# Kernel tuning notes

Hardware: AMD Instinct MI355X
Metric: run time of the kernel (lower is better)

The kernel has to match this reference:

```python
import jax, jax.numpy as jnp
import numpy as np

DIMVEC = 196
POS_LABEL = 98
NBLABELS = 10
M = 128
UNIHIGH = 0.012
BATCH = 8192


def setup_inputs() -> dict:
    key = jax.random.key(0)
    ks = jax.random.split(key, 6)
    # input features: one 2-vector per site, normalized to unit norm (cos/sin style)
    x = jax.random.uniform(ks[0], (BATCH, DIMVEC, 2), dtype=jnp.float32)
    x = x / jnp.linalg.norm(x, axis=-1, keepdims=True)
    # MPS tensors, uniform(0, unihigh) as in the original construct_tensornetwork
    w0 = jax.random.uniform(ks[1], (2, M), dtype=jnp.float32) * UNIHIGH
    w_left = jax.random.uniform(ks[2], (POS_LABEL - 1, 2, M, M), dtype=jnp.float32) * UNIHIGH
    w_label = jax.random.uniform(ks[3], (2, M, M, NBLABELS), dtype=jnp.float32) * UNIHIGH
    w_right = jax.random.uniform(ks[4], (DIMVEC - 2 - POS_LABEL, 2, M, M), dtype=jnp.float32) * UNIHIGH
    w_end = jax.random.uniform(ks[5], (2, M), dtype=jnp.float32) * UNIHIGH
    return {"x": x, "w0": w0, "w_left": w_left, "w_label": w_label,
            "w_right": w_right, "w_end": w_end}


def reference(x, w0, w_left, w_label, w_right, w_end):
    b, d, _ = x.shape
    m = w0.shape[1]

    # left boundary: contract physical leg of site 0 -> [B, m]
    left = x[:, 0, :] @ w0

    # sweep sites 1 .. pos_label-1: left'[b,n] = sum_{p,mm} x[b,p] left[b,mm] W[p,mm,n]
    def lstep(carry, inp):
        W, xi = inp                       # W: [2,m,m], xi: [B,2]
        o = (xi[:, :, None] * carry[:, None, :]).reshape(b, 2 * m)  # [B, 2m]
        return o @ W.reshape(2 * m, m), None                        # GEMM B x 2m x m

    left, _ = jax.lax.scan(lstep, left,
                           (w_left, jnp.swapaxes(x[:, 1:POS_LABEL], 0, 1)))

    # right boundary: contract physical leg of last site -> [B, m]
    right = x[:, -1, :] @ w_end

    # sweep sites dimvec-2 .. pos_label+1 (reverse):
    # right'[b,mm] = sum_{p,n} x[b,p] right[b,n] W[p,mm,n]
    def rstep(carry, inp):
        W, xi = inp
        o = (xi[:, :, None] * carry[:, None, :]).reshape(b, 2 * m)  # [B, 2m]
        Wt = jnp.swapaxes(W, 1, 2).reshape(2 * m, m)                # [p,n,mm] -> [2m, m]
        return o @ Wt, None

    right, _ = jax.lax.scan(rstep, right,
                            (w_right, jnp.swapaxes(x[:, POS_LABEL + 1:d - 1], 0, 1)),
                            reverse=True)

    # label site: contract left bond first (small intermediate [B,2,m,L])
    xl = x[:, POS_LABEL, :]                                   # [B, 2]
    z = jnp.einsum('bm,pmnl->bpnl', left, w_label)             # [B,2,m,L]
    leftL = jnp.einsum('bpnl,bp->bnl', z, xl)                  # [B,m,L]

    # close the chain with the right environment -> [B, nblabels]
    return jnp.einsum('bnl,bn->bl', leftL, right)
```

## Files before the change

kernel.cpp:

```cpp
#include <hip/hip_runtime.h>

#define BATCH 8192
#define MDIM 128
#define NL 10
#define LSTEPS 97
#define RSTEPS 96
#define NSTEPS 193
#define DIM 196
#define POSL 98

typedef _Float16 half8 __attribute__((ext_vector_type(8)));
typedef float float16v __attribute__((ext_vector_type(16)));

#define BARRIER_LGKM() asm volatile("s_waitcnt lgkmcnt(0)\ns_barrier" ::: "memory")

#define MFMA16 __builtin_amdgcn_mfma_f32_32x32x16_f16

__global__ __launch_bounds__(256) void transpose_x(const float* __restrict__ x,
                                                   float2* __restrict__ xT) {
    __shared__ float tx[64][65];
    __shared__ float ty[64][65];
    int p0 = blockIdx.x * 32;
    int b0 = blockIdx.y * 64;
    int tid = threadIdx.x;

    int r = tid >> 2, q = tid & 3;
    const float* src = x + ((size_t)(b0 + r) * DIM + p0 + q * 8) * 2;
#pragma unroll
    for (int j = 0; j < 8; ++j) {
        int pp = q * 8 + j;
        if (p0 + pp < DIM) {
            float2 v = *(const float2*)(src + j * 2);
            tx[r][pp] = v.x;
            ty[r][pp] = v.y;
        }
    }
    __syncthreads();

    int pr = tid >> 3, cb = (tid & 7) * 8;
    if (p0 + pr < DIM) {
        float2* dst = xT + (size_t)(p0 + pr) * BATCH + b0 + cb;
#pragma unroll
        for (int j = 0; j < 8; ++j) {
            float2 v;
            v.x = tx[cb + j][pr];
            v.y = ty[cb + j][pr];
            dst[j] = v;
        }
    }
}

__global__ __launch_bounds__(256) void pack_w(const float* __restrict__ w_left,
                                              const float* __restrict__ w_right,
                                              _Float16* __restrict__ pw) {
    int g = blockIdx.x >> 2;
    int nt = blockIdx.x & 3;
    int tid = threadIdx.x;
    int l = tid & 63;
    int kq = tid >> 6;
    int hi = l >> 5;
    int n = nt * 32 + (l & 31);
#pragma unroll
    for (int p = 0; p < 4; ++p) {
        int kt = p * 4 + kq;
        int k0 = kt * 16 + hi * 8;
        half8 hv;
        if (g < LSTEPS) {
            const float* base = w_left + (size_t)g * 2 * MDIM * MDIM;
#pragma unroll
            for (int j = 0; j < 8; ++j)
                hv[j] = (_Float16)base[(size_t)(k0 + j) * MDIM + n];
        } else {
            int t = g - LSTEPS;
            int s = k0 >> 7;
            int a0 = k0 & 127;
            const float* row = w_right + (size_t)(RSTEPS - 1 - t) * 2 * MDIM * MDIM
                             + (size_t)s * MDIM * MDIM + (size_t)n * MDIM + a0;
#pragma unroll
            for (int j = 0; j < 8; ++j) hv[j] = (_Float16)row[j];
        }
        *(half8*)(pw + (size_t)(g * 64 + nt * 16 + kt) * 512 + l * 8) = hv;
    }
}

__global__ __launch_bounds__(256) void pack_label(const float* __restrict__ w_label,
                                                  _Float16* __restrict__ gp) {
    int ct = blockIdx.x;
    int tid = threadIdx.x;
    int l = tid & 63;
    int kq = tid >> 6;
    int hi = l >> 5;
    int outcol = ct * 32 + (l & 31);
    int n = outcol & 127;
    int lab = outcol >> 7;
#pragma unroll
    for (int p2 = 0; p2 < 4; ++p2) {
        int kt = p2 * 4 + kq;
        int k0 = kt * 16 + hi * 8;
        int p = k0 >> 7;
        int m0 = k0 & 127;
        half8 hv;
#pragma unroll
        for (int j = 0; j < 8; ++j)
            hv[j] = (_Float16)w_label[(((size_t)p * MDIM + m0 + j) * MDIM + n) * NL + lab];
        *(half8*)(gp + (size_t)(ct * 16 + kt) * 512 + l * 8) = hv;
    }
}


#define LD16(dst, p, ofs) \
    asm volatile("global_load_dwordx4 %0, %1, off offset:" ofs : "=v"(dst) : "v"(p))

#define ISSUE_A(DST, PN) do {                                  \
    const char* _p0 = (PN);                                    \
    LD16(DST[0],  _p0, "0");                                   \
    LD16(DST[1],  _p0, "1024");                                \
    LD16(DST[2],  _p0, "2048");                                \
    LD16(DST[3],  _p0, "3072");                                \
    const char* _p1 = _p0 + 4096;                              \
    LD16(DST[4],  _p1, "0");                                   \
    LD16(DST[5],  _p1, "1024");                                \
    LD16(DST[6],  _p1, "2048");                                \
    LD16(DST[7],  _p1, "3072");                                \
    const char* _p2 = _p0 + 8192;                              \
    LD16(DST[8],  _p2, "0");                                   \
    LD16(DST[9],  _p2, "1024");                                \
    LD16(DST[10], _p2, "2048");                                \
    LD16(DST[11], _p2, "3072");                                \
    const char* _p3 = _p0 + 12288;                             \
    LD16(DST[12], _p3, "0");                                   \
    LD16(DST[13], _p3, "1024");                                \
    LD16(DST[14], _p3, "2048");                                \
    LD16(DST[15], _p3, "3072");                                \
} while (0)

#define WAIT_A16() do {                                        \
    asm volatile("s_waitcnt vmcnt(16)" ::: "memory");          \
    __builtin_amdgcn_sched_barrier(0);                         \
} while (0)

#define WAIT_A0() do {                                         \
    asm volatile("s_waitcnt vmcnt(0)" ::: "memory");           \
    __builtin_amdgcn_sched_barrier(0);                         \
} while (0)

#define CHAIN_MFMA_BLOCK(AF, SRC)                                            \
    half8 bf[8];                                                             \
    _Pragma("unroll")                                                        \
    for (int q = 0; q < 8; ++q) {                                            \
        int nb = q * 2 + hi;                                                 \
        int phys = nb ^ (bl & 15);                                           \
        bf[q] = *(const half8*)&cbuf[SRC][row * 128 + phys * 8];             \
    }                                                                        \
    float16v a0 = {}, a1 = {};                                               \
    _Pragma("unroll")                                                        \
    for (int kt = 0; kt < 8; ++kt) {                                         \
        a0 = MFMA16(AF[kt], bf[kt], a0, 0, 0, 0);                            \
        a1 = MFMA16(AF[kt + 8], bf[kt], a1, 0, 0, 0);                        \
    }

#define EPI_RG(DST, XC)                                                      \
    _Pragma("unroll")                                                        \
    for (int rq = 0; rq < 4; ++rq) {                                         \
        int nb = nt * 4 + rq;                                                \
        int phys = nb ^ (bl & 15);                                           \
        union { _Float16 h[4]; uint2 u; } t;                                 \
        _Pragma("unroll")                                                    \
        for (int r = 0; r < 4; ++r)                                          \
            t.h[r] = (_Float16)((XC).x * a0[rq * 4 + r]                      \
                              + (XC).y * a1[rq * 4 + r]);                    \
        *(uint2*)&cbuf[DST][row * 128 + phys * 8 + hi * 4] = t.u;            \
    }

#define FINAL_STORE(XC)                                                      \
    _Pragma("unroll")                                                        \
    for (int r = 0; r < 16; ++r) {                                           \
        int n = nt * 32 + (r & 3) + 8 * (r >> 2) + 4 * hi;                   \
        outT[(size_t)n * BATCH + bbase + row] = (XC).x * a0[r] + (XC).y * a1[r]; \
    }

__global__ __launch_bounds__(512, 2) void chain_mfma(
        const float2* __restrict__ xT, const float* __restrict__ w0,
        const float* __restrict__ w_end, const _Float16* __restrict__ pw,
        float* __restrict__ leftT, float* __restrict__ rightT) {
    __shared__ _Float16 cbuf[2][64 * 128];
    __shared__ float2 xbuf[98][64];

    int bid = blockIdx.x;
    bool is_left = bid < 128;
    int bbase = (is_left ? bid : bid - 128) * 64;
    int tid = threadIdx.x;
    int l = tid & 63;
    int w = tid >> 6;
    int nt = w & 3;
    int rg = w >> 2;
    int bl = l & 31;
    int hi = l >> 5;
    int row = rg * 32 + bl;

    int nsteps = is_left ? LSTEPS : RSTEPS;
    int gbase = is_left ? 0 : LSTEPS;
    int pbase = is_left ? 0 : 98;
    float* outT = is_left ? leftT : rightT;

    for (int i = tid; i < 98 * 64; i += 512) {
        int pos = i >> 6, b = i & 63;
        xbuf[pos][b] = xT[(size_t)(pbase + pos) * BATCH + bbase + b];
    }
    __syncthreads();

    {
        const float* wst = is_left ? w0 : w_end;
        int b = tid >> 3;
        float2 xv0 = xbuf[is_left ? 0 : 97][b];
#pragma unroll
        for (int h = 0; h < 2; ++h) {
            int nb = (tid & 7) * 2 + h;
            half8 hv;
#pragma unroll
            for (int j = 0; j < 8; ++j) {
                int n = nb * 8 + j;
                hv[j] = (_Float16)(xv0.x * wst[n] + xv0.y * wst[MDIM + n]);
            }
            int phys = nb ^ (b & 15);
            *(half8*)&cbuf[0][b * 128 + phys * 8] = hv;
        }
    }

    const char* pwb = (const char*)pw + (size_t)(gbase * 64 + nt * 16) * 1024
                    + (size_t)l * 16;

    __syncthreads();

    half8 A0[16], A1[16];
    ISSUE_A(A0, pwb);

    int npairs = nsteps >> 1;
    bool oddtail = nsteps & 1;
    int last = nsteps - 1;

#pragma unroll 1
    for (int sp = 0; sp < npairs; ++sp) {
        int s0 = 2 * sp;
        {
            ISSUE_A(A1, pwb + (size_t)(s0 + 1) * 65536);
            WAIT_A16();
            int xi = is_left ? (1 + s0) : (96 - s0);
            float2 xc = xbuf[xi][row];
            CHAIN_MFMA_BLOCK(A0, 0)
            EPI_RG(1, xc)
            BARRIER_LGKM();
        }
        {
            int s1 = s0 + 1;
            int pf = (s0 + 2 <= last) ? (s0 + 2) : last;
            ISSUE_A(A0, pwb + (size_t)pf * 65536);
            WAIT_A16();
            int xi = is_left ? (1 + s1) : (96 - s1);
            float2 xc = xbuf[xi][row];
            CHAIN_MFMA_BLOCK(A1, 1)
            if (s1 == last) {
                FINAL_STORE(xc)
            } else {
                EPI_RG(0, xc)
                BARRIER_LGKM();
            }
        }
    }

    if (oddtail) {
        WAIT_A0();
        float2 xc = xbuf[1 + last][row];
        CHAIN_MFMA_BLOCK(A0, 0)
        FINAL_STORE(xc)
    }
}

__global__ __launch_bounds__(256, 2) void label_mfma(
        const float2* __restrict__ xT, const _Float16* __restrict__ gp,
        const float* __restrict__ leftT, const float* __restrict__ rightT,
        float* __restrict__ out) {
    __shared__ _Float16 R[32 * 256];
    __shared__ float pl[4][32][5];
    __shared__ float xl_s[32][2];

    int bx = blockIdx.x;
    int bbase = blockIdx.y * 32;
    int tid = threadIdx.x;
    int l = tid & 63, nt = tid >> 6, bl = l & 31, hi = l >> 5;

    if (tid < 32) {
        const float2 v = xT[(size_t)POSL * BATCH + bbase + tid];
        xl_s[tid][0] = v.x; xl_s[tid][1] = v.y;
    }
    __syncthreads();

#pragma unroll
    for (int q = 0; q < 4; ++q) {
        int id = tid + q * 256;
        int m = id >> 3;
        int b4 = (id & 7) * 4;
        float4 v = *(const float4*)&leftT[(size_t)m * BATCH + bbase + b4];
        float vv[4] = {v.x, v.y, v.z, v.w};
#pragma unroll
        for (int bi = 0; bi < 4; ++bi) {
            int b = b4 + bi;
            int kb0 = m >> 3;
            int ph0 = (kb0 & 16) | ((kb0 ^ b) & 15);
            R[b * 256 + ph0 * 8 + (m & 7)] = (_Float16)(xl_s[b][0] * vv[bi]);
            int kb1 = kb0 + 16;
            int ph1 = (kb1 & 16) | ((kb1 ^ b) & 15);
            R[b * 256 + ph1 * 8 + (m & 7)] = (_Float16)(xl_s[b][1] * vv[bi]);
        }
    }

    float rv[16];
#pragma unroll
    for (int r = 0; r < 16; ++r) {
        int n = nt * 32 + (r & 3) + 8 * (r >> 2) + 4 * hi;
        rv[r] = rightT[(size_t)n * BATCH + bbase + bl];
    }
    __syncthreads();

    half8 rf[16];
#pragma unroll
    for (int kt = 0; kt < 16; ++kt) {
        int kb = kt * 2 + hi;
        int ph = (kb & 16) | ((kb ^ bl) & 15);
        rf[kt] = *(const half8*)&R[bl * 256 + ph * 8];
    }

    int l0 = bx * 5;
    float outv[5];
#pragma unroll
    for (int li = 0; li < 5; ++li) {
        int ct = (l0 + li) * 4 + nt;
        float16v acc = {};
#pragma unroll
        for (int kt = 0; kt < 16; ++kt) {
            half8 a = *(const half8*)(gp + (size_t)(ct * 16 + kt) * 512 + l * 8);
            acc = __builtin_amdgcn_mfma_f32_32x32x16_f16(a, rf[kt], acc, 0, 0, 0);
        }
        float p = 0.f;
#pragma unroll
        for (int r = 0; r < 16; ++r) p += acc[r] * rv[r];
        p += __shfl_xor(p, 32, 64);
        outv[li] = p;
    }
    if (hi == 0) {
#pragma unroll
        for (int li = 0; li < 5; ++li) pl[nt][bl][li] = outv[li];
    }
    __syncthreads();
    if (tid < 160) {
        int b = tid / 5, li = tid % 5;
        out[(size_t)(bbase + b) * NL + l0 + li] =
            pl[0][b][li] + pl[1][b][li] + pl[2][b][li] + pl[3][b][li];
    }
}

extern "C" void kernel_launch(void* const* d_in, const int* in_sizes, int n_in,
                              void* d_out, int out_size, void* d_ws, size_t ws_size,
                              hipStream_t stream) {
    const float* x       = (const float*)d_in[0];
    const float* w0      = (const float*)d_in[1];
    const float* w_left  = (const float*)d_in[2];
    const float* w_label = (const float*)d_in[3];
    const float* w_right = (const float*)d_in[4];
    const float* w_end   = (const float*)d_in[5];

    _Float16* pw = (_Float16*)d_ws;
    _Float16* gp = pw + (size_t)NSTEPS * 64 * 512;
    float* leftT  = (float*)(gp + (size_t)40 * 16 * 512);
    float* rightT = leftT + (size_t)MDIM * BATCH;
    float2* xT    = (float2*)(rightT + (size_t)MDIM * BATCH);

    transpose_x<<<dim3((DIM + 31) / 32, BATCH / 64), 256, 0, stream>>>(x, xT);
    pack_w<<<dim3(NSTEPS * 4), 256, 0, stream>>>(w_left, w_right, pw);
    pack_label<<<dim3(40), 256, 0, stream>>>(w_label, gp);
    chain_mfma<<<dim3(256), 512, 0, stream>>>(xT, w0, w_end, pw, leftT, rightT);
    label_mfma<<<dim3(2, BATCH / 32), 256, 0, stream>>>(xT, gp, leftT, rightT,
                                                        (float*)d_out);
}
```

Before: 253.9 us.

## Stream chain weights into LDS with global_load_lds double-buffered halves

Chain weight fragments no longer go straight into registers, where each wave loaded its own 16 fragments and the two row-group waves fetched the same data. The block now DMAs each step's weight tile into a double-buffered LDS area with global_load_lds, split into two K-halves, and waves read their fragments from LDS. This halves global weight traffic per block and cuts register pressure. The cost is extra barriers per step, extra LDS reads, and a much larger LDS footprint, which may limit residency to one block per CU.

```diff
diff --git a/kernel.cpp b/kernel.cpp
--- a/kernel.cpp
+++ b/kernel.cpp
@@ -13,8 +13,15 @@
 typedef float float16v __attribute__((ext_vector_type(16)));
 
 #define BARRIER_LGKM() asm volatile("s_waitcnt lgkmcnt(0)\ns_barrier" ::: "memory")
+#define BARRIER_PLAIN() asm volatile("s_barrier" ::: "memory")
+#define WAIT_VM4() asm volatile("s_waitcnt vmcnt(4)" ::: "memory")
 
 #define MFMA16 __builtin_amdgcn_mfma_f32_32x32x16_f16
+
+#define GLL16(G, L)                                                          \
+    __builtin_amdgcn_global_load_lds(                                        \
+        (const __attribute__((address_space(1))) unsigned int*)(G),          \
+        (__attribute__((address_space(3))) unsigned int*)(L), 16, 0, 0)
 
 __global__ __launch_bounds__(256) void transpose_x(const float* __restrict__ x,
                                                    float2* __restrict__ xT) {
@@ -108,56 +115,30 @@
 }
 
 
-#define LD16(dst, p, ofs) \
-    asm volatile("global_load_dwordx4 %0, %1, off offset:" ofs : "=v"(dst) : "v"(p))
-
-#define ISSUE_A(DST, PN) do {                                  \
-    const char* _p0 = (PN);                                    \
-    LD16(DST[0],  _p0, "0");                                   \
-    LD16(DST[1],  _p0, "1024");                                \
-    LD16(DST[2],  _p0, "2048");                                \
-    LD16(DST[3],  _p0, "3072");                                \
-    const char* _p1 = _p0 + 4096;                              \
-    LD16(DST[4],  _p1, "0");                                   \
-    LD16(DST[5],  _p1, "1024");                                \
-    LD16(DST[6],  _p1, "2048");                                \
-    LD16(DST[7],  _p1, "3072");                                \
-    const char* _p2 = _p0 + 8192;                              \
-    LD16(DST[8],  _p2, "0");                                   \
-    LD16(DST[9],  _p2, "1024");                                \
-    LD16(DST[10], _p2, "2048");                                \
-    LD16(DST[11], _p2, "3072");                                \
-    const char* _p3 = _p0 + 12288;                             \
-    LD16(DST[12], _p3, "0");                                   \
-    LD16(DST[13], _p3, "1024");                                \
-    LD16(DST[14], _p3, "2048");                                \
-    LD16(DST[15], _p3, "3072");                                \
+#define ISSUE_HALF(SRC_STEP, P, DST) do {                                    \
+    const char* _g = dmasrc + (size_t)(SRC_STEP) * 65536 + (P) * 8192;       \
+    GLL16(_g,        (DST));                                                 \
+    GLL16(_g + 1024, (DST) + 512);                                           \
+    GLL16(_g + 2048, (DST) + 1024);                                          \
+    GLL16(_g + 3072, (DST) + 1536);                                          \
 } while (0)
 
-#define WAIT_A16() do {                                        \
-    asm volatile("s_waitcnt vmcnt(16)" ::: "memory");          \
-    __builtin_amdgcn_sched_barrier(0);                         \
-} while (0)
-
-#define WAIT_A0() do {                                         \
-    asm volatile("s_waitcnt vmcnt(0)" ::: "memory");           \
-    __builtin_amdgcn_sched_barrier(0);                         \
-} while (0)
-
-#define CHAIN_MFMA_BLOCK(AF, SRC)                                            \
-    half8 bf[8];                                                             \
+#define READ_BF(SRC)                                                         \
     _Pragma("unroll")                                                        \
     for (int q = 0; q < 8; ++q) {                                            \
         int nb = q * 2 + hi;                                                 \
         int phys = nb ^ (bl & 15);                                           \
         bf[q] = *(const half8*)&cbuf[SRC][row * 128 + phys * 8];             \
-    }                                                                        \
-    float16v a0 = {}, a1 = {};                                               \
-    _Pragma("unroll")                                                        \
-    for (int kt = 0; kt < 8; ++kt) {                                         \
-        a0 = MFMA16(AF[kt], bf[kt], a0, 0, 0, 0);                            \
-        a1 = MFMA16(AF[kt + 8], bf[kt], a1, 0, 0, 0);                        \
-    }
+    }
+
+#define READ_AF(P)                                                           \
+    _Pragma("unroll")                                                        \
+    for (int f = 0; f < 8; ++f)                                              \
+        af[f] = *(const half8*)&ab[P][nt * 4096 + f * 512 + l * 8];
+
+#define MFMA_CHAIN(ACC)                                                      \
+    _Pragma("unroll")                                                        \
+    for (int f = 0; f < 8; ++f) ACC = MFMA16(af[f], bf[f], ACC, 0, 0, 0);
 
 #define EPI_RG(DST, XC)                                                      \
     _Pragma("unroll")                                                        \
@@ -183,6 +164,7 @@
         const float2* __restrict__ xT, const float* __restrict__ w0,
         const float* __restrict__ w_end, const _Float16* __restrict__ pw,
         float* __restrict__ leftT, float* __restrict__ rightT) {
+    __shared__ _Float16 ab[2][16384];
     __shared__ _Float16 cbuf[2][64 * 128];
     __shared__ float2 xbuf[98][64];
 
@@ -227,53 +209,50 @@
         }
     }
 
-    const char* pwb = (const char*)pw + (size_t)(gbase * 64 + nt * 16) * 1024
-                    + (size_t)l * 16;
-
-    __syncthreads();
-
-    half8 A0[16], A1[16];
-    ISSUE_A(A0, pwb);
-
-    int npairs = nsteps >> 1;
-    bool oddtail = nsteps & 1;
+    const char* dmasrc = (const char*)pw + (size_t)gbase * 65536
+                       + (size_t)(w >> 1) * 16384 + (size_t)(w & 1) * 4096
+                       + (size_t)l * 16;
+    _Float16* dmadst0 = &ab[0][w * 2048];
+    _Float16* dmadst1 = &ab[1][w * 2048];
+
+    ISSUE_HALF(0, 0, dmadst0);
+    ISSUE_HALF(0, 1, dmadst1);
+    WAIT_VM4();
+    BARRIER_LGKM();
+
     int last = nsteps - 1;
 
 #pragma unroll 1
-    for (int sp = 0; sp < npairs; ++sp) {
-        int s0 = 2 * sp;
-        {
-            ISSUE_A(A1, pwb + (size_t)(s0 + 1) * 65536);
-            WAIT_A16();
-            int xi = is_left ? (1 + s0) : (96 - s0);
-            float2 xc = xbuf[xi][row];
-            CHAIN_MFMA_BLOCK(A0, 0)
-            EPI_RG(1, xc)
+    for (int s = 0; s < nsteps; ++s) {
+        int d = s & 1;
+        int xi = is_left ? (1 + s) : (96 - s);
+        int pf = (s < last) ? (s + 1) : last;
+
+        half8 bf[8], af[8];
+        READ_BF(d)
+        float2 xc = xbuf[xi][row];
+        READ_AF(0)
+        float16v a0 = {};
+        MFMA_CHAIN(a0)
+        BARRIER_LGKM();
+        ISSUE_HALF(pf, 0, dmadst0);
+        WAIT_VM4();
+        BARRIER_PLAIN();
+        READ_AF(1)
+        float16v a1 = {};
+        MFMA_CHAIN(a1)
+        if (s == last) {
+            FINAL_STORE(xc)
+        } else {
+            EPI_RG(d ^ 1, xc)
             BARRIER_LGKM();
-        }
-        {
-            int s1 = s0 + 1;
-            int pf = (s0 + 2 <= last) ? (s0 + 2) : last;
-            ISSUE_A(A0, pwb + (size_t)pf * 65536);
-            WAIT_A16();
-            int xi = is_left ? (1 + s1) : (96 - s1);
-            float2 xc = xbuf[xi][row];
-            CHAIN_MFMA_BLOCK(A1, 1)
-            if (s1 == last) {
-                FINAL_STORE(xc)
-            } else {
-                EPI_RG(0, xc)
-                BARRIER_LGKM();
-            }
-        }
-    }
-
-    if (oddtail) {
-        WAIT_A0();
-        float2 xc = xbuf[1 + last][row];
-        CHAIN_MFMA_BLOCK(A0, 0)
-        FINAL_STORE(xc)
-    }
+            ISSUE_HALF(pf, 1, dmadst1);
+            WAIT_VM4();
+            BARRIER_PLAIN();
+        }
+    }
+
+    asm volatile("s_waitcnt vmcnt(0)" ::: "memory");
 }
 
 __global__ __launch_bounds__(256, 2) void label_mfma(
```

New measurement: 279.7 us. 1.1x slower.
